# Optimization experiments

Hardware: AMD Instinct MI355X
Metric: run time of the kernel (lower is better)

## Reference

```python
import jax, jax.numpy as jnp
import numpy as np

EMBED_DIM = 1024
HEAD_SIZE = 64
B, T = 4, 4096


def setup_inputs() -> dict:
    key = jax.random.key(0)
    kx, kq, kk, kv = jax.random.split(key, 4)
    x = jax.random.normal(kx, (B, T, EMBED_DIM), dtype=jnp.float32)
    sw = 1.0 / np.sqrt(EMBED_DIM)  # kaiming-ish init scale for linear weights
    Wq = jax.random.normal(kq, (EMBED_DIM, HEAD_SIZE), dtype=jnp.float32) * sw
    Wk = jax.random.normal(kk, (EMBED_DIM, HEAD_SIZE), dtype=jnp.float32) * sw
    Wv = jax.random.normal(kv, (EMBED_DIM, HEAD_SIZE), dtype=jnp.float32) * sw
    return {"x": x, "Wq": Wq, "Wk": Wk, "Wv": Wv}


def reference(x, Wq, Wk, Wv):
    Bn, Tn, C = x.shape
    q = jnp.einsum('btc,ch->bth', x, Wq)
    k = jnp.einsum('btc,ch->bth', x, Wk)
    v = jnp.einsum('btc,ch->bth', x, Wv)
    # NOTE: original scales by sqrt(C) = sqrt(embed_dim), not sqrt(head_size)
    scale = 1.0 / jnp.sqrt(jnp.asarray(C, dtype=x.dtype))
    wei = jnp.einsum('bth,bsh->bts', q, k) * scale  # [B, T, T]
    causal = jnp.tril(jnp.ones((Tn, Tn), dtype=bool))
    wei = jnp.where(causal, wei, -jnp.inf)
    wei = jax.nn.softmax(wei, axis=-1)
    # dropout p=0.0 (eval mode): identity
    return jnp.einsum('bts,bsh->bth', wei, v)
```

## Files before the change

kernel.cpp:

```cpp
#include <hip/hip_runtime.h>
#include <cstdint>


typedef __bf16 bf16;
typedef __bf16 bf16x4 __attribute__((ext_vector_type(4)));
typedef __bf16 bf16x8 __attribute__((ext_vector_type(8)));
typedef float  f32x4  __attribute__((ext_vector_type(4)));

#define MFMA16(a, b, c) __builtin_amdgcn_mfma_f32_16x16x32_bf16((a), (b), (c), 0, 0, 0)

#if __has_builtin(__builtin_amdgcn_exp2f)
#define EXP2(x) __builtin_amdgcn_exp2f(x)
#else
#define EXP2(x) exp2f(x)
#endif

#define B_SZ 4
#define T_SZ 4096
#define C_SZ 1024
#define H_SZ 64
#define M_SZ (B_SZ * T_SZ)
#define QSCALE (1.4426950408889634f / 32.0f)
#define P_O 8192
#define P_L 128

__device__ __forceinline__ void dma16(const void* g, void* l) {
    __builtin_amdgcn_global_load_lds(
        (const __attribute__((address_space(1))) uint32_t*)(uintptr_t)g,
        (__attribute__((address_space(3))) uint32_t*)(uint32_t)(uintptr_t)l,
        16, 0, 0);
}

#define WAIT_BARRIER(N) do {                                       \
    asm volatile("s_waitcnt vmcnt(" #N ")" ::: "memory");          \
    __builtin_amdgcn_s_barrier();                                  \
    __builtin_amdgcn_sched_barrier(0);                             \
} while (0)

#define BOT_BARRIER() do {                                         \
    __builtin_amdgcn_sched_barrier(0);                             \
    __builtin_amdgcn_s_barrier();                                  \
    __builtin_amdgcn_sched_barrier(0);                             \
} while (0)

__global__ __launch_bounds__(256) void wt_prep(
    const float* __restrict__ Wq, const float* __restrict__ Wk,
    const float* __restrict__ Wv, bf16* __restrict__ wt2)
{
    const int n4 = blockIdx.x, t = threadIdx.x;
    const int nbase = n4 * 4;
    const float* W = (nbase < 64) ? Wq : (nbase < 128 ? Wk : Wv);
    const float sc = (nbase < 64) ? QSCALE : 1.0f;
    const int ncol = nbase & 63;
    #pragma unroll
    for (int i = 0; i < 4; ++i) {
        const int k = i * 256 + t;
        const float4 v = *(const float4*)(W + (size_t)k * H_SZ + ncol);
        const float vals[4] = {v.x, v.y, v.z, v.w};
        const size_t base = (size_t)(k >> 6) * 12288 + (size_t)((k >> 5) & 1) * 6144
                          + (size_t)((k >> 3) & 3) * 1536 + (k & 7);
        #pragma unroll
        for (int m = 0; m < 4; ++m)
            wt2[base + (size_t)(nbase + m) * 8] = (bf16)(vals[m] * sc);
    }
}

__global__ __launch_bounds__(256) void qkv_proj(
    const float* __restrict__ x, const bf16* __restrict__ wt2,
    bf16* __restrict__ qw, bf16* __restrict__ kw2, bf16* __restrict__ vtw2)
{
    const int m0 = blockIdx.x * 32;
    const int tid = threadIdx.x;
    const int wave = tid >> 6, lane = tid & 63;
    const int quad = lane >> 4, l15 = lane & 15;
    const int phase = blockIdx.x & 15;

    __shared__ __align__(16) float xs[2][2 * 4 * 32 * 8];
    __shared__ __align__(16) bf16  ws[2][2 * 4 * 192 * 8];

    f32x4 acc[2][3] = {};

    const char* xg = (const char*)x
        + (size_t)(m0 + ((tid >> 1) & 31)) * 4096
        + (size_t)((tid >> 6) & 3) * 32 + (size_t)(tid & 1) * 16;
    const char* wg = (const char*)wt2 + (size_t)tid * 16;

    auto stage = [&](int s, int buf) {
        const size_t se = (size_t)((s + phase) & 15);
        char* xl = (char*)(&xs[buf][0]) + (size_t)tid * 16;
        char* wl = (char*)(&ws[buf][0]) + (size_t)tid * 16;
        dma16(xg + se * 256, xl);
        dma16(xg + se * 256 + 128, xl + 4096);
        #pragma unroll
        for (int i = 0; i < 6; ++i)
            dma16(wg + se * 24576 + (size_t)i * 4096, wl + (size_t)i * 4096);
    };

    stage(0, 0);

    for (int s = 0; s < 16; ++s) {
        if (s < 15) {
            stage(s + 1, (s + 1) & 1);
            WAIT_BARRIER(8);
        } else {
            WAIT_BARRIER(0);
        }
        const float* xb = &xs[s & 1][0];
        const bf16*  wb = &ws[s & 1][0];

        #pragma unroll
        for (int ss = 0; ss < 2; ++ss) {
            bf16x8 a[2];
            #pragma unroll
            for (int mg = 0; mg < 2; ++mg) {
                const float* ap = xb + ss * 1024 + quad * 256 + (mg * 16 + l15) * 8;
                const f32x4 lo = *(const f32x4*)ap;
                const f32x4 hi = *(const f32x4*)(ap + 4);
                a[mg][0] = (bf16)lo[0]; a[mg][1] = (bf16)lo[1];
                a[mg][2] = (bf16)lo[2]; a[mg][3] = (bf16)lo[3];
                a[mg][4] = (bf16)hi[0]; a[mg][5] = (bf16)hi[1];
                a[mg][6] = (bf16)hi[2]; a[mg][7] = (bf16)hi[3];
            }
            #pragma unroll
            for (int i = 0; i < 3; ++i) {
                const int nt = wave * 3 + i;
                const bf16x8 wf = *(const bf16x8*)(wb + ss * 6144 + quad * 1536
                                                   + (nt * 16 + l15) * 8);
                #pragma unroll
                for (int mg = 0; mg < 2; ++mg)
                    acc[mg][i] = MFMA16(a[mg], wf, acc[mg][i]);
            }
        }

        BOT_BARRIER();
    }

    #pragma unroll
    for (int mg = 0; mg < 2; ++mg)
        #pragma unroll
        for (int i = 0; i < 3; ++i) {
            const int n = (wave * 3 + i) * 16 + l15;
            const int which = n >> 6, col = n & 63;
            #pragma unroll
            for (int r = 0; r < 4; ++r) {
                const int t = m0 + mg * 16 + quad * 4 + r;
                const bf16 v = (bf16)acc[mg][i][r];
                if (which == 0) {
                    qw[(size_t)t * H_SZ + col] = v;
                } else if (which == 1) {
                    kw2[(size_t)(t >> 6) * 4096
                        + (size_t)(((col >> 5) << 2) + ((col >> 3) & 3)) * 512
                        + (size_t)(t & 63) * 8 + (col & 7)] = v;
                } else {
                    const int t6 = t & 63;
                    const int p = ((t6 >> 2) & 3) * 8 + (t6 & 3) * 2
                                + ((t6 >> 4) & 1) + (t6 >> 5) * 32;
                    vtw2[(size_t)(t >> 6) * 4096
                         + (size_t)(p >> 3) * 512 + (size_t)col * 8 + (p & 7)] = v;
                }
            }
        }
}

__global__ __launch_bounds__(256) void flash_attn(
    const bf16* __restrict__ qw, const bf16* __restrict__ kw2,
    const bf16* __restrict__ vtw2, bf16* __restrict__ pbuf_o,
    float* __restrict__ pbuf_l)
{
    const int bx = blockIdx.x;
    const int item = (bx & 1) ? (511 - (bx >> 1)) : (bx >> 1);
    const int qt2 = 31 - (item >> 4);
    const int b   = (item >> 2) & 3;
    const int h   = item & 3;
    const int i0  = qt2 * 128;
    const int nkv = qt2 * 2 + 2;

    const int tid = threadIdx.x;
    const int wave = tid >> 6, lane = tid & 63;
    const int quad = lane >> 4, l15 = lane & 15;

    __shared__ __align__(16) bf16 kvs[2][8192];

    bf16x8 aq[2][2];
    #pragma unroll
    for (int mg2 = 0; mg2 < 2; ++mg2) {
        const bf16* qp = qw + ((size_t)b * T_SZ + i0 + wave * 32 + mg2 * 16 + l15) * H_SZ
                       + quad * 8;
        aq[mg2][0] = *(const bf16x8*)qp;
        aq[mg2][1] = *(const bf16x8*)(qp + 32);
    }
    const bf16 onev = (bf16)1.0f;
    const bf16x8 vone = {onev, onev, onev, onev, onev, onev, onev, onev};

    const char* kgb = (const char*)kw2 + (size_t)b * 524288;
    const char* vgb = (const char*)vtw2 + (size_t)b * 524288;

    f32x4 o[2][4] = {};
    f32x4 osum[2] = {};

    auto stage = [&](int jt, int buf) {
        const char* ks = kgb + (size_t)jt * 8192;
        const char* vs = vgb + (size_t)jt * 8192;
        char* dst = (char*)(&kvs[buf][0]) + (size_t)tid * 16;
        dma16(ks + (size_t)tid * 16, dst);
        dma16(ks + 4096 + (size_t)tid * 16, dst + 4096);
        dma16(vs + (size_t)tid * 16, dst + 8192);
        dma16(vs + 4096 + (size_t)tid * 16, dst + 12288);
    };

    if (h < nkv) stage(h, 0);

    int c = 0;
    for (int jt = h; jt < nkv; jt += 4, c ^= 1) {
        if (jt + 4 < nkv) {
            stage(jt + 4, c ^ 1);
            WAIT_BARRIER(4);
        } else {
            WAIT_BARRIER(0);
        }
        const bf16* kb = &kvs[c][0];
        const bf16* vb = &kvs[c][0] + 4096;

        f32x4 s4t[4][2] = {};
        __builtin_amdgcn_s_setprio(1);
        #pragma unroll
        for (int ct = 0; ct < 4; ++ct) {
            const bf16x8 k0 = *(const bf16x8*)(kb + (0 * 4 + quad) * 512 + (ct * 16 + l15) * 8);
            const bf16x8 k1 = *(const bf16x8*)(kb + (1 * 4 + quad) * 512 + (ct * 16 + l15) * 8);
            #pragma unroll
            for (int mg2 = 0; mg2 < 2; ++mg2) {
                s4t[ct][mg2] = MFMA16(k0, aq[mg2][0], s4t[ct][mg2]);
                s4t[ct][mg2] = MFMA16(k1, aq[mg2][1], s4t[ct][mg2]);
            }
        }
        __builtin_amdgcn_s_setprio(0);

        if (jt >= 2 * qt2) {
            #pragma unroll
            for (int mg2 = 0; mg2 < 2; ++mg2) {
                const int gq = i0 + wave * 32 + mg2 * 16 + l15;
                #pragma unroll
                for (int ct = 0; ct < 4; ++ct) {
                    const int gkv0 = jt * 64 + ct * 16 + quad * 4;
                    #pragma unroll
                    for (int rr = 0; rr < 4; ++rr)
                        if (gkv0 + rr > gq) s4t[ct][mg2][rr] = -3.0e38f;
                }
            }
        }

        bf16x8 pa[2][2];
        #pragma unroll
        for (int mg2 = 0; mg2 < 2; ++mg2)
            #pragma unroll
            for (int j = 0; j < 8; ++j) {
                pa[mg2][0][j] = (bf16)EXP2(s4t[j & 1][mg2][j >> 1]);
                pa[mg2][1][j] = (bf16)EXP2(s4t[2 + (j & 1)][mg2][j >> 1]);
            }

        __builtin_amdgcn_s_setprio(1);
        #pragma unroll
        for (int ht = 0; ht < 4; ++ht) {
            const bf16x8 v0 = *(const bf16x8*)(vb + (0 * 4 + quad) * 512 + (ht * 16 + l15) * 8);
            const bf16x8 v1 = *(const bf16x8*)(vb + (1 * 4 + quad) * 512 + (ht * 16 + l15) * 8);
            #pragma unroll
            for (int mg2 = 0; mg2 < 2; ++mg2) {
                o[mg2][ht] = MFMA16(pa[mg2][0], v0, o[mg2][ht]);
                o[mg2][ht] = MFMA16(pa[mg2][1], v1, o[mg2][ht]);
            }
        }
        #pragma unroll
        for (int mg2 = 0; mg2 < 2; ++mg2) {
            osum[mg2] = MFMA16(pa[mg2][0], vone, osum[mg2]);
            osum[mg2] = MFMA16(pa[mg2][1], vone, osum[mg2]);
        }
        __builtin_amdgcn_s_setprio(0);

        BOT_BARRIER();
    }

    bf16* pb_o = pbuf_o + (size_t)(((b * 32 + qt2) * 4) + h) * P_O;
    float* pb_l = pbuf_l + (size_t)(((b * 32 + qt2) * 4) + h) * P_L;
    #pragma unroll
    for (int mg2 = 0; mg2 < 2; ++mg2) {
        const int L0 = wave * 32 + mg2 * 16 + quad * 4;
        #pragma unroll
        for (int ht = 0; ht < 4; ++ht)
            #pragma unroll
            for (int rr = 0; rr < 4; ++rr)
                pb_o[(L0 + rr) * 64 + ht * 16 + l15] = (bf16)o[mg2][ht][rr];
        if (l15 == 0) {
            #pragma unroll
            for (int rr = 0; rr < 4; ++rr)
                pb_l[L0 + rr] = osum[mg2][rr];
        }
    }
}

__global__ __launch_bounds__(256) void combine(
    const bf16* __restrict__ pbuf_o, const float* __restrict__ pbuf_l,
    float* __restrict__ out)
{
    const int bq2 = blockIdx.x >> 1, tid = threadIdx.x;
    const int row = ((blockIdx.x & 1) << 6) + (tid >> 2);
    const int c0 = (tid & 3) * 16;

    float a[16] = {};
    float l = 0.f;
    #pragma unroll
    for (int h = 0; h < 4; ++h) {
        const bf16* ph = pbuf_o + (size_t)(bq2 * 4 + h) * P_O + row * 64 + c0;
        const bf16x8 v0 = *(const bf16x8*)ph;
        const bf16x8 v1 = *(const bf16x8*)(ph + 8);
        #pragma unroll
        for (int j = 0; j < 8; ++j) {
            a[j]     += (float)v0[j];
            a[8 + j] += (float)v1[j];
        }
        l += pbuf_l[(size_t)(bq2 * 4 + h) * P_L + row];
    }
    const float inv = 1.0f / l;
    float* op = out + ((size_t)bq2 * 128 + row) * 64 + c0;
    #pragma unroll
    for (int g = 0; g < 4; ++g) {
        f32x4 v = {a[g * 4], a[g * 4 + 1], a[g * 4 + 2], a[g * 4 + 3]};
        *(f32x4*)(op + g * 4) = v * inv;
    }
}

extern "C" void kernel_launch(void* const* d_in, const int* in_sizes, int n_in,
                              void* d_out, int out_size, void* d_ws, size_t ws_size,
                              hipStream_t stream) {
    const float* x  = (const float*)d_in[0];
    const float* Wq = (const float*)d_in[1];
    const float* Wk = (const float*)d_in[2];
    const float* Wv = (const float*)d_in[3];

    bf16* qw   = (bf16*)d_ws;
    bf16* kw2  = qw + (size_t)M_SZ * H_SZ;
    bf16* vtw2 = kw2 + (size_t)M_SZ * H_SZ;
    bf16* wt2  = vtw2 + (size_t)M_SZ * H_SZ;
    bf16* pbuf_o = wt2 + 3 * 64 * 1024;
    float* pbuf_l = (float*)(pbuf_o + (size_t)512 * P_O);
    float* out = (float*)d_out;

    wt_prep<<<48, 256, 0, stream>>>(Wq, Wk, Wv, wt2);
    qkv_proj<<<M_SZ / 32, 256, 0, stream>>>(x, wt2, qw, kw2, vtw2);
    flash_attn<<<512, 256, 0, stream>>>(qw, kw2, vtw2, pbuf_o, pbuf_l);
    combine<<<256, 256, 0, stream>>>(pbuf_o, pbuf_l, out);
}
```

Before: 141.2 us.

## Fuse split-KV combine into flash attention via last-block atomic counter

Removes the separate combine kernel. Each attention block writes its partial output, then bumps an atomic counter for its query-tile group, and the fourth block to arrive sums the partials and writes the normalized output. The last block uses its own partials straight from registers. This saves a kernel launch and one pass over the partial buffers, at the cost of a threadfence, an atomic and extra serialized work in the tail block of each group. The counters are reset in wt_prep.

```diff
diff --git a/kernel.cpp b/kernel.cpp
--- a/kernel.cpp
+++ b/kernel.cpp
@@ -45,9 +45,11 @@
 
 __global__ __launch_bounds__(256) void wt_prep(
     const float* __restrict__ Wq, const float* __restrict__ Wk,
-    const float* __restrict__ Wv, bf16* __restrict__ wt2)
+    const float* __restrict__ Wv, bf16* __restrict__ wt2,
+    int* __restrict__ cnt)
 {
     const int n4 = blockIdx.x, t = threadIdx.x;
+    if (n4 == 0 && t < 128) cnt[t] = 0;
     const int nbase = n4 * 4;
     const float* W = (nbase < 64) ? Wq : (nbase < 128 ? Wk : Wv);
     const float sc = (nbase < 64) ? QSCALE : 1.0f;
@@ -165,7 +167,8 @@
 __global__ __launch_bounds__(256) void flash_attn(
     const bf16* __restrict__ qw, const bf16* __restrict__ kw2,
     const bf16* __restrict__ vtw2, bf16* __restrict__ pbuf_o,
-    float* __restrict__ pbuf_l)
+    float* __restrict__ pbuf_l, int* __restrict__ cnt,
+    float* __restrict__ out)
 {
     const int bx = blockIdx.x;
     const int item = (bx & 1) ? (511 - (bx >> 1)) : (bx >> 1);
@@ -279,8 +282,9 @@
         BOT_BARRIER();
     }
 
-    bf16* pb_o = pbuf_o + (size_t)(((b * 32 + qt2) * 4) + h) * P_O;
-    float* pb_l = pbuf_l + (size_t)(((b * 32 + qt2) * 4) + h) * P_L;
+    const int grp = b * 32 + qt2;
+    bf16* pb_o = pbuf_o + (size_t)(grp * 4 + h) * P_O;
+    float* pb_l = pbuf_l + (size_t)(grp * 4 + h) * P_L;
     #pragma unroll
     for (int mg2 = 0; mg2 < 2; ++mg2) {
         const int L0 = wave * 32 + mg2 * 16 + quad * 4;
@@ -295,36 +299,45 @@
                 pb_l[L0 + rr] = osum[mg2][rr];
         }
     }
-}
-
-__global__ __launch_bounds__(256) void combine(
-    const bf16* __restrict__ pbuf_o, const float* __restrict__ pbuf_l,
-    float* __restrict__ out)
-{
-    const int bq2 = blockIdx.x >> 1, tid = threadIdx.x;
-    const int row = ((blockIdx.x & 1) << 6) + (tid >> 2);
-    const int c0 = (tid & 3) * 16;
-
-    float a[16] = {};
-    float l = 0.f;
-    #pragma unroll
-    for (int h = 0; h < 4; ++h) {
-        const bf16* ph = pbuf_o + (size_t)(bq2 * 4 + h) * P_O + row * 64 + c0;
-        const bf16x8 v0 = *(const bf16x8*)ph;
-        const bf16x8 v1 = *(const bf16x8*)(ph + 8);
-        #pragma unroll
-        for (int j = 0; j < 8; ++j) {
-            a[j]     += (float)v0[j];
-            a[8 + j] += (float)v1[j];
-        }
-        l += pbuf_l[(size_t)(bq2 * 4 + h) * P_L + row];
-    }
-    const float inv = 1.0f / l;
-    float* op = out + ((size_t)bq2 * 128 + row) * 64 + c0;
-    #pragma unroll
-    for (int g = 0; g < 4; ++g) {
-        f32x4 v = {a[g * 4], a[g * 4 + 1], a[g * 4 + 2], a[g * 4 + 3]};
-        *(f32x4*)(op + g * 4) = v * inv;
+
+    __shared__ int last_flag;
+    __threadfence();
+    __syncthreads();
+    if (tid == 0) {
+        const int t = __hip_atomic_fetch_add(&cnt[grp], 1, __ATOMIC_ACQ_REL,
+                                             __HIP_MEMORY_SCOPE_AGENT);
+        last_flag = (t == 3);
+    }
+    __syncthreads();
+    if (!last_flag) return;
+    __threadfence();
+
+    const bf16* gb_o = pbuf_o + (size_t)(grp * 4) * P_O;
+    const float* gb_l = pbuf_l + (size_t)(grp * 4) * P_L;
+    float* ob = out + ((size_t)b * T_SZ + i0) * H_SZ;
+    #pragma unroll
+    for (int mg2 = 0; mg2 < 2; ++mg2) {
+        const int L0 = wave * 32 + mg2 * 16 + quad * 4;
+        float inv[4];
+        #pragma unroll
+        for (int rr = 0; rr < 4; ++rr) {
+            float ls = osum[mg2][rr];
+            #pragma unroll
+            for (int hh = 0; hh < 4; ++hh)
+                if (hh != h) ls += gb_l[(size_t)hh * P_L + L0 + rr];
+            inv[rr] = 1.0f / ls;
+        }
+        #pragma unroll
+        for (int ht = 0; ht < 4; ++ht)
+            #pragma unroll
+            for (int rr = 0; rr < 4; ++rr) {
+                float v = o[mg2][ht][rr];
+                #pragma unroll
+                for (int hh = 0; hh < 4; ++hh)
+                    if (hh != h)
+                        v += (float)gb_o[(size_t)hh * P_O + (L0 + rr) * 64 + ht * 16 + l15];
+                ob[(size_t)(L0 + rr) * H_SZ + ht * 16 + l15] = v * inv[rr];
+            }
     }
 }
 
@@ -342,10 +355,10 @@
     bf16* wt2  = vtw2 + (size_t)M_SZ * H_SZ;
     bf16* pbuf_o = wt2 + 3 * 64 * 1024;
     float* pbuf_l = (float*)(pbuf_o + (size_t)512 * P_O);
+    int* cnt = (int*)(pbuf_l + (size_t)512 * P_L);
     float* out = (float*)d_out;
 
-    wt_prep<<<48, 256, 0, stream>>>(Wq, Wk, Wv, wt2);
+    wt_prep<<<48, 256, 0, stream>>>(Wq, Wk, Wv, wt2, cnt);
     qkv_proj<<<M_SZ / 32, 256, 0, stream>>>(x, wt2, qw, kw2, vtw2);
-    flash_attn<<<512, 256, 0, stream>>>(qw, kw2, vtw2, pbuf_o, pbuf_l);
-    combine<<<256, 256, 0, stream>>>(pbuf_o, pbuf_l, out);
-}
+    flash_attn<<<512, 256, 0, stream>>>(qw, kw2, vtw2, pbuf_o, pbuf_l, cnt, out);
+}
```

New measurement: 238.6 us. 69.0% more time.
